# Kernel optimization log

Measured on AMD Instinct MI355X. Metric: run time of the kernel, lower is better.

## Reference

```python
import jax, jax.numpy as jnp
import numpy as np

N_NODES = 100000
N_EDGES = 800000
IN_DIM, HID_DIM, OUT_DIM = 128, 64, 7


def setup_inputs() -> dict:
    key = jax.random.key(0)
    ks = jax.random.split(key, 8)
    x = jax.random.normal(ks[0], (N_NODES, IN_DIM), dtype=jnp.float32)
    edge_index = jax.random.randint(ks[1], (2, N_EDGES), 0, N_NODES, dtype=jnp.int64)
    # Glorot-ish init for weights, zeros for bias (PyG GCNConv default)
    def glorot(k, shape):
        lim = float(np.sqrt(6.0 / (shape[0] + shape[1])))
        return jax.random.uniform(k, shape, dtype=jnp.float32, minval=-lim, maxval=lim)
    return {
        "x": x,
        "edge_index": edge_index,
        "W1": glorot(ks[2], (IN_DIM, HID_DIM)),
        "b1": jnp.zeros((HID_DIM,), jnp.float32),
        "W2": glorot(ks[3], (HID_DIM, HID_DIM)),
        "b2": jnp.zeros((HID_DIM,), jnp.float32),
        "W3": glorot(ks[4], (HID_DIM, OUT_DIM)),
        "b3": jnp.zeros((OUT_DIM,), jnp.float32),
    }


def _gcn_conv(h_in, src, dst, W, b, n_nodes):
    # PyG GCNConv: h = x @ W; add self-loops; D^-1/2 A_hat D^-1/2 aggregation; + b
    h = h_in @ W  # [N, F_out]
    # degree over destination nodes, +1 for self-loop
    deg = jax.ops.segment_sum(jnp.ones_like(dst, dtype=h.dtype), dst,
                              num_segments=n_nodes) + 1.0
    dinv = jax.lax.rsqrt(deg)  # [N]
    coef = dinv[src] * dinv[dst]  # [E]
    msg = h[src] * coef[:, None]  # gather + scale  [E, F_out]
    out = jax.ops.segment_sum(msg, dst, num_segments=n_nodes)  # scatter-add
    out = out + h * (dinv * dinv)[:, None]  # self-loop contribution
    return out + b


def reference(x, edge_index, W1, b1, W2, b2, W3, b3):
    src, dst = edge_index[0], edge_index[1]
    n = x.shape[0]
    h = jax.nn.relu(_gcn_conv(x, src, dst, W1, b1, n))
    # dropout(p=0.5) is identity in eval mode
    h = jax.nn.relu(_gcn_conv(h, src, dst, W2, b2, n))
    return _gcn_conv(h, src, dst, W3, b3, n)
```

## Files before the change

### kernel.cpp

```cpp
#include <hip/hip_runtime.h>

#define N_NODES 100000
#define N_EDGES 800000
#define IN_DIM 128
#define HID 64
#define OUT_DIM 7
#define CAP 32
#define NGROUP 8
#define DSLICE (N_NODES / NGROUP)
#define SUBBLK 390
#define NB_N ((N_NODES + 255) / 256)

typedef __bf16 vbf8 __attribute__((ext_vector_type(8)));
typedef float  vf4  __attribute__((ext_vector_type(4)));

__device__ __forceinline__ void wswz_body(int idx, const float* __restrict__ W,
                                          __bf16* __restrict__ out) {
    int j  = idx & 7;
    int l  = (idx >> 3) & 63;
    int nt = (idx >> 9) & 3;
    int ks = idx >> 11;
    int k  = ks * 32 + ((l >> 4) << 3) + j;
    int n  = nt * 16 + (l & 15);
    out[idx] = (__bf16)W[k * 64 + n];
}

__global__ __launch_bounds__(256)
void k_init(const float* __restrict__ W1, __bf16* __restrict__ Wz1,
            const float* __restrict__ W2, __bf16* __restrict__ Wz2,
            __bf16* __restrict__ HbA, __bf16* __restrict__ HbB,
            float* __restrict__ S) {
    int b = blockIdx.x;
    int t = threadIdx.x;
    if (b < 32) { wswz_body(b * 256 + t, W1, Wz1); return; }
    if (b < 48) { wswz_body((b - 32) * 256 + t, W2, Wz2); return; }
    if (t < 32)       ((unsigned*)(HbA + (size_t)N_NODES * 64))[t] = 0u;
    else if (t < 64)  ((unsigned*)(HbB + (size_t)N_NODES * 64))[t - 32] = 0u;
    else if (t < 71)  S[(size_t)N_NODES * 7 + (t - 64)] = 0.0f;
}

__device__ __forceinline__ void gemm1_body(int g, int tid, const float* __restrict__ X,
                                           const __bf16* __restrict__ Wswz,
                                           __bf16* __restrict__ Hb) {
    constexpr int K = IN_DIM, KS = K / 32;
    const int lane = tid & 63;
    const int w = g * 4 + (tid >> 6);
    if (w >= N_NODES / 16) return;
    const int r0 = w * 16;
    const int m = lane & 15;
    const int quad = lane >> 4;

    vbf8 bfrag[KS][4];
    const vbf8* wp = (const vbf8*)Wswz;
    #pragma unroll
    for (int ks = 0; ks < KS; ++ks)
        #pragma unroll
        for (int nt = 0; nt < 4; ++nt)
            bfrag[ks][nt] = wp[(ks * 4 + nt) * 64 + lane];

    vf4 acc[4] = {};
    #pragma unroll
    for (int ks = 0; ks < KS; ++ks) {
        const float* xp = X + (size_t)(r0 + m) * K + ks * 32 + quad * 8;
        float4 f0 = *(const float4*)xp;
        float4 f1 = *(const float4*)(xp + 4);
        vbf8 a;
        a[0] = (__bf16)f0.x; a[1] = (__bf16)f0.y; a[2] = (__bf16)f0.z; a[3] = (__bf16)f0.w;
        a[4] = (__bf16)f1.x; a[5] = (__bf16)f1.y; a[6] = (__bf16)f1.z; a[7] = (__bf16)f1.w;
        #pragma unroll
        for (int nt = 0; nt < 4; ++nt)
            acc[nt] = __builtin_amdgcn_mfma_f32_16x16x32_bf16(a, bfrag[ks][nt], acc[nt], 0, 0, 0);
    }
    #pragma unroll
    for (int nt = 0; nt < 4; ++nt)
        #pragma unroll
        for (int r = 0; r < 4; ++r)
            Hb[(size_t)(r0 + quad * 4 + r) * 64 + nt * 16 + m] = (__bf16)acc[nt][r];
}

#define FILL_BLKS (NGROUP * SUBBLK)
#define GEMM_BLKS ((N_NODES / 16 + 3) / 4)
__global__ __launch_bounds__(256)
void k_build_gemm1(const int* __restrict__ ei, int* __restrict__ cnt,
                   int* __restrict__ csr, const float* __restrict__ X,
                   const __bf16* __restrict__ Wz1, __bf16* __restrict__ Hb) {
    int b = blockIdx.x;
    if (b < GEMM_BLKS) {
        gemm1_body(b, threadIdx.x, X, Wz1, Hb);
    } else {
        int bb = b - GEMM_BLKS;
        int group = bb & 7, sub = bb >> 3;
        int lo = group * DSLICE;
        const int4* dst4 = (const int4*)(ei + N_EDGES);
        const int4* src4 = (const int4*)ei;
        for (int e4 = sub * 256 + threadIdx.x; e4 < N_EDGES / 4; e4 += SUBBLK * 256) {
            int4 d4 = dst4[e4];
            int4 s4 = src4[e4];
            bool m0 = (unsigned)(d4.x - lo) < (unsigned)DSLICE;
            bool m1 = (unsigned)(d4.y - lo) < (unsigned)DSLICE;
            bool m2 = (unsigned)(d4.z - lo) < (unsigned)DSLICE;
            bool m3 = (unsigned)(d4.w - lo) < (unsigned)DSLICE;
            if (!(m0 | m1 | m2 | m3)) continue;
            if (m0) { int p = atomicAdd(&cnt[d4.x], 1); if (p < CAP) csr[(size_t)d4.x * CAP + p] = s4.x; }
            if (m1) { int p = atomicAdd(&cnt[d4.y], 1); if (p < CAP) csr[(size_t)d4.y * CAP + p] = s4.y; }
            if (m2) { int p = atomicAdd(&cnt[d4.z], 1); if (p < CAP) csr[(size_t)d4.z * CAP + p] = s4.z; }
            if (m3) { int p = atomicAdd(&cnt[d4.w], 1); if (p < CAP) csr[(size_t)d4.w * CAP + p] = s4.w; }
        }
    }
}

__global__ __launch_bounds__(256)
void k_scale(const int* __restrict__ cnt, __bf16* __restrict__ Hb) {
    int idx = (blockIdx.x * 256 + threadIdx.x) * 8;
    int row = idx >> 6;
    float dinv = rsqrtf((float)cnt[row] + 1.0f);
    vbf8 v = *(const vbf8*)(Hb + idx);
    #pragma unroll
    for (int t = 0; t < 8; ++t) v[t] = (__bf16)((float)v[t] * dinv);
    *(vbf8*)(Hb + idx) = v;
}

__global__ __launch_bounds__(256)
void k_gemm2(const __bf16* __restrict__ Ab, const __bf16* __restrict__ Wz2,
             const int* __restrict__ cnt, __bf16* __restrict__ Hb) {
    constexpr int KS = 2;
    const int tid = threadIdx.x;
    const int lane = tid & 63;
    const int w = blockIdx.x * 4 + (tid >> 6);
    if (w >= N_NODES / 16) return;
    const int r0 = w * 16;
    const int m = lane & 15;
    const int quad = lane >> 4;

    vbf8 bfrag[KS][4];
    const vbf8* wp = (const vbf8*)Wz2;
    #pragma unroll
    for (int ks = 0; ks < KS; ++ks)
        #pragma unroll
        for (int nt = 0; nt < 4; ++nt)
            bfrag[ks][nt] = wp[(ks * 4 + nt) * 64 + lane];

    vf4 acc[4] = {};
    #pragma unroll
    for (int ks = 0; ks < KS; ++ks) {
        vbf8 a = *(const vbf8*)(Ab + (size_t)(r0 + m) * 64 + ks * 32 + quad * 8);
        #pragma unroll
        for (int nt = 0; nt < 4; ++nt)
            acc[nt] = __builtin_amdgcn_mfma_f32_16x16x32_bf16(a, bfrag[ks][nt], acc[nt], 0, 0, 0);
    }
    float dv[4];
    #pragma unroll
    for (int r = 0; r < 4; ++r)
        dv[r] = rsqrtf((float)cnt[r0 + quad * 4 + r] + 1.0f);
    #pragma unroll
    for (int nt = 0; nt < 4; ++nt)
        #pragma unroll
        for (int r = 0; r < 4; ++r)
            Hb[(size_t)(r0 + quad * 4 + r) * 64 + nt * 16 + m] = (__bf16)(acc[nt][r] * dv[r]);
}

__global__ __launch_bounds__(256)
void k_gather64(const int* __restrict__ cnt, const int* __restrict__ csr,
                const float* __restrict__ bias, const __bf16* __restrict__ Hs,
                __bf16* __restrict__ Ab) {
    int node = blockIdx.x * 32 + (threadIdx.x >> 3);
    int q = threadIdx.x & 7;
    if (node >= N_NODES) return;
    int deg = cnt[node];
    int end = deg < CAP ? deg : CAP;
    float dd = rsqrtf((float)deg + 1.0f);
    vbf8 h8 = *(const vbf8*)(Hs + (size_t)node * 64 + q * 8);
    float acc[8];
    #pragma unroll
    for (int t = 0; t < 8; ++t) acc[t] = (float)h8[t];

    const int4* row4 = (const int4*)(csr + (size_t)node * CAP);
    int4 qa = row4[0], qb = row4[1], qc = row4[2], qd = row4[3];
    int srcs[16] = {qa.x, qa.y, qa.z, qa.w, qb.x, qb.y, qb.z, qb.w,
                    qc.x, qc.y, qc.z, qc.w, qd.x, qd.y, qd.z, qd.w};
    #pragma unroll
    for (int t = 0; t < 16; ++t) {
        int s = (t < end) ? srcs[t] : N_NODES;
        vbf8 v = *(const vbf8*)(Hs + (size_t)s * 64 + q * 8);
        #pragma unroll
        for (int u = 0; u < 8; ++u) acc[u] += (float)v[u];
    }
    for (int j = 16; j < end; ++j) {
        int s = (csr + (size_t)node * CAP)[j];
        vbf8 v = *(const vbf8*)(Hs + (size_t)s * 64 + q * 8);
        #pragma unroll
        for (int u = 0; u < 8; ++u) acc[u] += (float)v[u];
    }
    float4 b0 = *(const float4*)(bias + q * 8);
    float4 b1 = *(const float4*)(bias + q * 8 + 4);
    float bb[8] = {b0.x, b0.y, b0.z, b0.w, b1.x, b1.y, b1.z, b1.w};
    vbf8 o;
    #pragma unroll
    for (int t = 0; t < 8; ++t) o[t] = (__bf16)fmaxf(fmaf(acc[t], dd, bb[t]), 0.f);
    *(vbf8*)(Ab + (size_t)node * 64 + q * 8) = o;
}

__global__ __launch_bounds__(256)
void k_gather64m(const int* __restrict__ cnt, const int* __restrict__ csr,
                 const float* __restrict__ bias, const __bf16* __restrict__ Hs,
                 const float* __restrict__ W3, float* __restrict__ S) {
    int node = blockIdx.x * 32 + (threadIdx.x >> 3);
    int q = threadIdx.x & 7;
    if (node >= N_NODES) return;
    int deg = cnt[node];
    int end = deg < CAP ? deg : CAP;
    float dd = rsqrtf((float)deg + 1.0f);
    vbf8 h8 = *(const vbf8*)(Hs + (size_t)node * 64 + q * 8);
    float acc[8];
    #pragma unroll
    for (int t = 0; t < 8; ++t) acc[t] = (float)h8[t];

    const int4* row4 = (const int4*)(csr + (size_t)node * CAP);
    int4 qa = row4[0], qb = row4[1], qc = row4[2], qd = row4[3];
    int srcs[16] = {qa.x, qa.y, qa.z, qa.w, qb.x, qb.y, qb.z, qb.w,
                    qc.x, qc.y, qc.z, qc.w, qd.x, qd.y, qd.z, qd.w};
    #pragma unroll
    for (int t = 0; t < 16; ++t) {
        int s = (t < end) ? srcs[t] : N_NODES;
        vbf8 v = *(const vbf8*)(Hs + (size_t)s * 64 + q * 8);
        #pragma unroll
        for (int u = 0; u < 8; ++u) acc[u] += (float)v[u];
    }
    for (int j = 16; j < end; ++j) {
        int s = (csr + (size_t)node * CAP)[j];
        vbf8 v = *(const vbf8*)(Hs + (size_t)s * 64 + q * 8);
        #pragma unroll
        for (int u = 0; u < 8; ++u) acc[u] += (float)v[u];
    }

    float4 b0 = *(const float4*)(bias + q * 8);
    float4 b1 = *(const float4*)(bias + q * 8 + 4);
    float bb[8] = {b0.x, b0.y, b0.z, b0.w, b1.x, b1.y, b1.z, b1.w};
    float p[7] = {};
    #pragma unroll
    for (int t = 0; t < 8; ++t) {
        float r = fmaxf(fmaf(acc[t], dd, bb[t]), 0.f);
        #pragma unroll
        for (int j = 0; j < 7; ++j)
            p[j] = fmaf(r, W3[(q * 8 + t) * 7 + j], p[j]);
    }
    #pragma unroll
    for (int msk = 1; msk < 8; msk <<= 1)
        #pragma unroll
        for (int j = 0; j < 7; ++j)
            p[j] += __shfl_xor(p[j], msk, 8);
    if (q < 7) {
        float v = p[0];
        if (q == 1) v = p[1]; else if (q == 2) v = p[2]; else if (q == 3) v = p[3];
        else if (q == 4) v = p[4]; else if (q == 5) v = p[5]; else if (q == 6) v = p[6];
        S[(size_t)node * 7 + q] = v * dd;
    }
}

__global__ __launch_bounds__(256)
void k_gather7(const int* __restrict__ cnt, const int* __restrict__ csr,
               const float* __restrict__ S, const float* __restrict__ b3,
               float* __restrict__ Out) {
    int node = blockIdx.x * 32 + (threadIdx.x >> 3);
    int j7 = threadIdx.x & 7;
    if (node >= N_NODES || j7 >= 7) return;
    int deg = cnt[node];
    int end = deg < CAP ? deg : CAP;
    float dd = rsqrtf((float)deg + 1.0f);
    const int4* row4 = (const int4*)(csr + (size_t)node * CAP);
    int4 qa = row4[0], qb = row4[1], qc = row4[2], qd = row4[3];
    int srcs[16] = {qa.x, qa.y, qa.z, qa.w, qb.x, qb.y, qb.z, qb.w,
                    qc.x, qc.y, qc.z, qc.w, qd.x, qd.y, qd.z, qd.w};
    float acc = S[(size_t)node * 7 + j7];
    #pragma unroll
    for (int t = 0; t < 16; ++t) {
        int s = (t < end) ? srcs[t] : N_NODES;
        acc += S[(size_t)s * 7 + j7];
    }
    for (int j = 16; j < end; ++j) {
        int s = (csr + (size_t)node * CAP)[j];
        acc += S[(size_t)s * 7 + j7];
    }
    Out[(size_t)node * 7 + j7] = fmaf(acc, dd, b3[j7]);
}

static inline size_t align256(size_t x) { return (x + 255) & ~(size_t)255; }

extern "C" void kernel_launch(void* const* d_in, const int* in_sizes, int n_in,
                              void* d_out, int out_size, void* d_ws, size_t ws_size,
                              hipStream_t stream) {
    const float* x  = (const float*)d_in[0];
    const int*   ei = (const int*)d_in[1];
    const float* W1 = (const float*)d_in[2];
    const float* b1 = (const float*)d_in[3];
    const float* W2 = (const float*)d_in[4];
    const float* b2 = (const float*)d_in[5];
    const float* W3 = (const float*)d_in[6];
    const float* b3 = (const float*)d_in[7];
    float* out = (float*)d_out;

    char* wsp = (char*)d_ws;
    int*    cnt  = (int*)wsp;    wsp += align256(sizeof(int) * N_NODES);
    int*    csr  = (int*)wsp;    wsp += align256(sizeof(int) * (size_t)N_NODES * CAP);
    __bf16* Wz1  = (__bf16*)wsp; wsp += align256(sizeof(__bf16) * IN_DIM * 64);
    __bf16* Wz2  = (__bf16*)wsp; wsp += align256(sizeof(__bf16) * HID * 64);
    __bf16* HbA  = (__bf16*)wsp; wsp += align256(sizeof(__bf16) * (size_t)(N_NODES + 1) * 64);
    __bf16* Ab   = (__bf16*)wsp; wsp += align256(sizeof(__bf16) * (size_t)N_NODES * 64);
    __bf16* HbB  = (__bf16*)wsp; wsp += align256(sizeof(__bf16) * (size_t)(N_NODES + 1) * 64);
    float*  bufS = (float*)wsp;  wsp += align256(sizeof(float) * (size_t)(N_NODES + 1) * 7);

    hipMemsetAsync(cnt, 0, sizeof(int) * N_NODES, stream);
    k_init<<<49, 256, 0, stream>>>(W1, Wz1, W2, Wz2, HbA, HbB, bufS);
    k_build_gemm1<<<GEMM_BLKS + FILL_BLKS, 256, 0, stream>>>(ei, cnt, csr, x, Wz1, HbA);
    k_scale<<<(N_NODES * 64) / (8 * 256), 256, 0, stream>>>(cnt, HbA);
    k_gather64<<<N_NODES / 32, 256, 0, stream>>>(cnt, csr, b1, HbA, Ab);
    k_gemm2<<<GEMM_BLKS, 256, 0, stream>>>(Ab, Wz2, cnt, HbB);
    k_gather64m<<<N_NODES / 32, 256, 0, stream>>>(cnt, csr, b2, HbB, W3, bufS);
    k_gather7<<<N_NODES / 32, 256, 0, stream>>>(cnt, csr, bufS, b3, out);
}
```

Before: 205.5 us.

## Fold source-degree scaling into first gather and drop separate scale kernel

Removes the k_scale pass over the layer-1 feature matrix. The first gather now multiplies each neighbour row by its own rsqrt-degree, read from cnt, and the self term by the node's degree; cnt gets a padding slot so the dummy index N_NODES is safe. It also hoists the X loads in gemm1 ahead of the weight-fragment loads, adds an occupancy hint to the build/gemm1 kernel, and delays the src load in the CSR fill until a destination matches. The trade-off is an extra scattered cnt load and rsqrt per gathered edge in exchange for one fewer full read-write pass over the feature matrix.

```diff
diff --git a/kernel.cpp b/kernel.cpp
--- a/kernel.cpp
+++ b/kernel.cpp
@@ -50,6 +50,14 @@
     const int m = lane & 15;
     const int quad = lane >> 4;
 
+    const float* xp = X + (size_t)(r0 + m) * K + quad * 8;
+    float4 f0[KS], f1[KS];
+    #pragma unroll
+    for (int ks = 0; ks < KS; ++ks) {
+        f0[ks] = *(const float4*)(xp + ks * 32);
+        f1[ks] = *(const float4*)(xp + ks * 32 + 4);
+    }
+
     vbf8 bfrag[KS][4];
     const vbf8* wp = (const vbf8*)Wswz;
     #pragma unroll
@@ -61,12 +69,11 @@
     vf4 acc[4] = {};
     #pragma unroll
     for (int ks = 0; ks < KS; ++ks) {
-        const float* xp = X + (size_t)(r0 + m) * K + ks * 32 + quad * 8;
-        float4 f0 = *(const float4*)xp;
-        float4 f1 = *(const float4*)(xp + 4);
         vbf8 a;
-        a[0] = (__bf16)f0.x; a[1] = (__bf16)f0.y; a[2] = (__bf16)f0.z; a[3] = (__bf16)f0.w;
-        a[4] = (__bf16)f1.x; a[5] = (__bf16)f1.y; a[6] = (__bf16)f1.z; a[7] = (__bf16)f1.w;
+        a[0] = (__bf16)f0[ks].x; a[1] = (__bf16)f0[ks].y;
+        a[2] = (__bf16)f0[ks].z; a[3] = (__bf16)f0[ks].w;
+        a[4] = (__bf16)f1[ks].x; a[5] = (__bf16)f1[ks].y;
+        a[6] = (__bf16)f1[ks].z; a[7] = (__bf16)f1[ks].w;
         #pragma unroll
         for (int nt = 0; nt < 4; ++nt)
             acc[nt] = __builtin_amdgcn_mfma_f32_16x16x32_bf16(a, bfrag[ks][nt], acc[nt], 0, 0, 0);
@@ -80,7 +87,7 @@
 
 #define FILL_BLKS (NGROUP * SUBBLK)
 #define GEMM_BLKS ((N_NODES / 16 + 3) / 4)
-__global__ __launch_bounds__(256)
+__global__ __launch_bounds__(256, 4)
 void k_build_gemm1(const int* __restrict__ ei, int* __restrict__ cnt,
                    int* __restrict__ csr, const float* __restrict__ X,
                    const __bf16* __restrict__ Wz1, __bf16* __restrict__ Hb) {
@@ -95,68 +102,18 @@
         const int4* src4 = (const int4*)ei;
         for (int e4 = sub * 256 + threadIdx.x; e4 < N_EDGES / 4; e4 += SUBBLK * 256) {
             int4 d4 = dst4[e4];
-            int4 s4 = src4[e4];
             bool m0 = (unsigned)(d4.x - lo) < (unsigned)DSLICE;
             bool m1 = (unsigned)(d4.y - lo) < (unsigned)DSLICE;
             bool m2 = (unsigned)(d4.z - lo) < (unsigned)DSLICE;
             bool m3 = (unsigned)(d4.w - lo) < (unsigned)DSLICE;
             if (!(m0 | m1 | m2 | m3)) continue;
+            int4 s4 = src4[e4];
             if (m0) { int p = atomicAdd(&cnt[d4.x], 1); if (p < CAP) csr[(size_t)d4.x * CAP + p] = s4.x; }
             if (m1) { int p = atomicAdd(&cnt[d4.y], 1); if (p < CAP) csr[(size_t)d4.y * CAP + p] = s4.y; }
             if (m2) { int p = atomicAdd(&cnt[d4.z], 1); if (p < CAP) csr[(size_t)d4.z * CAP + p] = s4.z; }
             if (m3) { int p = atomicAdd(&cnt[d4.w], 1); if (p < CAP) csr[(size_t)d4.w * CAP + p] = s4.w; }
         }
     }
-}
-
-__global__ __launch_bounds__(256)
-void k_scale(const int* __restrict__ cnt, __bf16* __restrict__ Hb) {
-    int idx = (blockIdx.x * 256 + threadIdx.x) * 8;
-    int row = idx >> 6;
-    float dinv = rsqrtf((float)cnt[row] + 1.0f);
-    vbf8 v = *(const vbf8*)(Hb + idx);
-    #pragma unroll
-    for (int t = 0; t < 8; ++t) v[t] = (__bf16)((float)v[t] * dinv);
-    *(vbf8*)(Hb + idx) = v;
-}
-
-__global__ __launch_bounds__(256)
-void k_gemm2(const __bf16* __restrict__ Ab, const __bf16* __restrict__ Wz2,
-             const int* __restrict__ cnt, __bf16* __restrict__ Hb) {
-    constexpr int KS = 2;
-    const int tid = threadIdx.x;
-    const int lane = tid & 63;
-    const int w = blockIdx.x * 4 + (tid >> 6);
-    if (w >= N_NODES / 16) return;
-    const int r0 = w * 16;
-    const int m = lane & 15;
-    const int quad = lane >> 4;
-
-    vbf8 bfrag[KS][4];
-    const vbf8* wp = (const vbf8*)Wz2;
-    #pragma unroll
-    for (int ks = 0; ks < KS; ++ks)
-        #pragma unroll
-        for (int nt = 0; nt < 4; ++nt)
-            bfrag[ks][nt] = wp[(ks * 4 + nt) * 64 + lane];
-
-    vf4 acc[4] = {};
-    #pragma unroll
-    for (int ks = 0; ks < KS; ++ks) {
-        vbf8 a = *(const vbf8*)(Ab + (size_t)(r0 + m) * 64 + ks * 32 + quad * 8);
-        #pragma unroll
-        for (int nt = 0; nt < 4; ++nt)
-            acc[nt] = __builtin_amdgcn_mfma_f32_16x16x32_bf16(a, bfrag[ks][nt], acc[nt], 0, 0, 0);
-    }
-    float dv[4];
-    #pragma unroll
-    for (int r = 0; r < 4; ++r)
-        dv[r] = rsqrtf((float)cnt[r0 + quad * 4 + r] + 1.0f);
-    #pragma unroll
-    for (int nt = 0; nt < 4; ++nt)
-        #pragma unroll
-        for (int r = 0; r < 4; ++r)
-            Hb[(size_t)(r0 + quad * 4 + r) * 64 + nt * 16 + m] = (__bf16)(acc[nt][r] * dv[r]);
 }
 
 __global__ __launch_bounds__(256)
@@ -172,7 +129,7 @@
     vbf8 h8 = *(const vbf8*)(Hs + (size_t)node * 64 + q * 8);
     float acc[8];
     #pragma unroll
-    for (int t = 0; t < 8; ++t) acc[t] = (float)h8[t];
+    for (int t = 0; t < 8; ++t) acc[t] = (float)h8[t] * dd;
 
     const int4* row4 = (const int4*)(csr + (size_t)node * CAP);
     int4 qa = row4[0], qb = row4[1], qc = row4[2], qd = row4[3];
@@ -181,15 +138,17 @@
     #pragma unroll
     for (int t = 0; t < 16; ++t) {
         int s = (t < end) ? srcs[t] : N_NODES;
+        float ds = rsqrtf((float)cnt[s] + 1.0f);
         vbf8 v = *(const vbf8*)(Hs + (size_t)s * 64 + q * 8);
         #pragma unroll
-        for (int u = 0; u < 8; ++u) acc[u] += (float)v[u];
+        for (int u = 0; u < 8; ++u) acc[u] += (float)v[u] * ds;
     }
     for (int j = 16; j < end; ++j) {
         int s = (csr + (size_t)node * CAP)[j];
+        float ds = rsqrtf((float)cnt[s] + 1.0f);
         vbf8 v = *(const vbf8*)(Hs + (size_t)s * 64 + q * 8);
         #pragma unroll
-        for (int u = 0; u < 8; ++u) acc[u] += (float)v[u];
+        for (int u = 0; u < 8; ++u) acc[u] += (float)v[u] * ds;
     }
     float4 b0 = *(const float4*)(bias + q * 8);
     float4 b1 = *(const float4*)(bias + q * 8 + 4);
@@ -198,6 +157,45 @@
     #pragma unroll
     for (int t = 0; t < 8; ++t) o[t] = (__bf16)fmaxf(fmaf(acc[t], dd, bb[t]), 0.f);
     *(vbf8*)(Ab + (size_t)node * 64 + q * 8) = o;
+}
+
+__global__ __launch_bounds__(256)
+void k_gemm2(const __bf16* __restrict__ Ab, const __bf16* __restrict__ Wz2,
+             const int* __restrict__ cnt, __bf16* __restrict__ Hb) {
+    constexpr int KS = 2;
+    const int tid = threadIdx.x;
+    const int lane = tid & 63;
+    const int w = blockIdx.x * 4 + (tid >> 6);
+    if (w >= N_NODES / 16) return;
+    const int r0 = w * 16;
+    const int m = lane & 15;
+    const int quad = lane >> 4;
+
+    vbf8 bfrag[KS][4];
+    const vbf8* wp = (const vbf8*)Wz2;
+    #pragma unroll
+    for (int ks = 0; ks < KS; ++ks)
+        #pragma unroll
+        for (int nt = 0; nt < 4; ++nt)
+            bfrag[ks][nt] = wp[(ks * 4 + nt) * 64 + lane];
+
+    vf4 acc[4] = {};
+    #pragma unroll
+    for (int ks = 0; ks < KS; ++ks) {
+        vbf8 a = *(const vbf8*)(Ab + (size_t)(r0 + m) * 64 + ks * 32 + quad * 8);
+        #pragma unroll
+        for (int nt = 0; nt < 4; ++nt)
+            acc[nt] = __builtin_amdgcn_mfma_f32_16x16x32_bf16(a, bfrag[ks][nt], acc[nt], 0, 0, 0);
+    }
+    float dv[4];
+    #pragma unroll
+    for (int r = 0; r < 4; ++r)
+        dv[r] = rsqrtf((float)cnt[r0 + quad * 4 + r] + 1.0f);
+    #pragma unroll
+    for (int nt = 0; nt < 4; ++nt)
+        #pragma unroll
+        for (int r = 0; r < 4; ++r)
+            Hb[(size_t)(r0 + quad * 4 + r) * 64 + nt * 16 + m] = (__bf16)(acc[nt][r] * dv[r]);
 }
 
 __global__ __launch_bounds__(256)
@@ -300,7 +298,7 @@
     float* out = (float*)d_out;
 
     char* wsp = (char*)d_ws;
-    int*    cnt  = (int*)wsp;    wsp += align256(sizeof(int) * N_NODES);
+    int*    cnt  = (int*)wsp;    wsp += align256(sizeof(int) * (N_NODES + 1));
     int*    csr  = (int*)wsp;    wsp += align256(sizeof(int) * (size_t)N_NODES * CAP);
     __bf16* Wz1  = (__bf16*)wsp; wsp += align256(sizeof(__bf16) * IN_DIM * 64);
     __bf16* Wz2  = (__bf16*)wsp; wsp += align256(sizeof(__bf16) * HID * 64);
@@ -309,10 +307,9 @@
     __bf16* HbB  = (__bf16*)wsp; wsp += align256(sizeof(__bf16) * (size_t)(N_NODES + 1) * 64);
     float*  bufS = (float*)wsp;  wsp += align256(sizeof(float) * (size_t)(N_NODES + 1) * 7);
 
-    hipMemsetAsync(cnt, 0, sizeof(int) * N_NODES, stream);
+    hipMemsetAsync(cnt, 0, sizeof(int) * (N_NODES + 1), stream);
     k_init<<<49, 256, 0, stream>>>(W1, Wz1, W2, Wz2, HbA, HbB, bufS);
     k_build_gemm1<<<GEMM_BLKS + FILL_BLKS, 256, 0, stream>>>(ei, cnt, csr, x, Wz1, HbA);
-    k_scale<<<(N_NODES * 64) / (8 * 256), 256, 0, stream>>>(cnt, HbA);
     k_gather64<<<N_NODES / 32, 256, 0, stream>>>(cnt, csr, b1, HbA, Ab);
     k_gemm2<<<GEMM_BLKS, 256, 0, stream>>>(Ab, Wz2, cnt, HbB);
     k_gather64m<<<N_NODES / 32, 256, 0, stream>>>(cnt, csr, b2, HbB, W3, bufS);
```

Measured after the change: 207.7 us. About the same (+1.0%).
